# Kernel tuning notes

Measured on AMD Instinct MI355X. Metric: run time of the kernel, lower is better.

Reference implementation:

```python
import jax, jax.numpy as jnp
import numpy as np

B, S, D, H = 2, 2048, 1024, 16
HD = D // H            # head_dim = 64
CHUNK = 1024           # hard-coded in the torch module
ROPE_THETA = 10000.0


def setup_inputs() -> dict:
    key = jax.random.key(0)
    ks = jax.random.split(key, 5)
    hidden_states = jax.random.normal(ks[0], (B, S, D), dtype=jnp.float32)
    # Precomputed RoPE frequencies: freqs_cis[s, j] = exp(i * s * theta_j),
    # stored as real [S, HD//2, 2] = (cos, sin).
    inv_freq = 1.0 / (ROPE_THETA ** (np.arange(0, HD, 2, dtype=np.float32) / HD))
    ang = np.outer(np.arange(S, dtype=np.float32), inv_freq)  # [S, HD//2]
    freqs_cis = jnp.stack([jnp.cos(ang), jnp.sin(ang)], axis=-1).astype(jnp.float32)
    scale = 0.02
    Wq = jax.random.normal(ks[1], (D, D), dtype=jnp.float32) * scale
    Wk = jax.random.normal(ks[2], (D, D), dtype=jnp.float32) * scale
    Wv = jax.random.normal(ks[3], (D, D), dtype=jnp.float32) * scale
    Wo = jax.random.normal(ks[4], (D, D), dtype=jnp.float32) * scale
    return {"hidden_states": hidden_states, "freqs_cis": freqs_cis,
            "Wq": Wq, "Wk": Wk, "Wv": Wv, "Wo": Wo}


def _apply_rope(x, freqs_cis):
    # x: [B, S, H, HD]; freqs_cis: [S, HD//2, 2] (cos, sin)
    b, s, h, hd = x.shape
    xr = x.reshape(b, s, h, hd // 2, 2)
    a, bb = xr[..., 0], xr[..., 1]
    c = freqs_cis[:s, :, 0][None, :, None, :]  # broadcast over batch, heads
    d = freqs_cis[:s, :, 1][None, :, None, :]
    # complex multiply (a + ib)(c + id)
    out = jnp.stack([a * c - bb * d, a * d + bb * c], axis=-1)
    return out.reshape(b, s, h, hd)


def reference(hidden_states, freqs_cis, Wq, Wk, Wv, Wo):
    b, s, dm = hidden_states.shape
    q = (hidden_states @ Wq).reshape(b, s, H, HD)
    k = (hidden_states @ Wk).reshape(b, s, H, HD)
    v = (hidden_states @ Wv).reshape(b, s, H, HD)
    q = _apply_rope(q, freqs_cis)
    k = _apply_rope(k, freqs_cis)
    q = q.transpose(0, 2, 1, 3)  # [B, H, S, HD]
    k = k.transpose(0, 2, 1, 3)
    v = v.transpose(0, 2, 1, 3)
    scaling = HD ** (-0.5)
    out = jnp.zeros_like(q)
    # Faithful replication of the (buggy) chunked attention: softmax is
    # normalized PER key-chunk, then chunk outputs are summed.
    for i in range(0, s, CHUNK):
        j = min(i + CHUNK, s)
        w = jnp.einsum('bhqd,bhkd->bhqk', q, k[:, :, i:j]) * scaling
        w = jax.nn.softmax(w.astype(jnp.float32), axis=-1).astype(q.dtype)
        out = out + jnp.einsum('bhqk,bhkd->bhqd', w, v[:, :, i:j])
    out = out.transpose(0, 2, 1, 3).reshape(b, s, dm)
    return out @ Wo
```

## Files before the change

kernel.cpp:

```cpp
#include <hip/hip_runtime.h>
#include <hip/hip_bf16.h>
#include <cstdint>

typedef __bf16 bf16x8 __attribute__((ext_vector_type(8)));
typedef float f32x4 __attribute__((ext_vector_type(4)));
typedef float f32x16 __attribute__((ext_vector_type(16)));

#define MFMA16(a, b, c) __builtin_amdgcn_mfma_f32_16x16x32_bf16(a, b, c, 0, 0, 0)
#define MFMA32(a, b, c) __builtin_amdgcn_mfma_f32_32x32x16_bf16(a, b, c, 0, 0, 0)

__device__ __forceinline__ void gload_lds16(const void* g, void* l) {
  __builtin_amdgcn_global_load_lds(
      (const __attribute__((address_space(1))) unsigned int*)g,
      (__attribute__((address_space(3))) unsigned int*)l, 16, 0, 0);
}

__device__ __forceinline__ unsigned short f2bf(float x) {
  union { float f; uint32_t u; } v; v.f = x;
  uint32_t r = v.u + 0x7fff + ((v.u >> 16) & 1);
  return (unsigned short)(r >> 16);
}
__device__ __forceinline__ float bf2f(unsigned short h) {
  union { float f; uint32_t u; } v; v.u = ((uint32_t)h) << 16;
  return v.f;
}
__device__ __forceinline__ f32x16 fzero16() {
  f32x16 v;
#pragma unroll
  for (int i = 0; i < 16; ++i) v[i] = 0.f;
  return v;
}

__device__ __forceinline__ void ptrans(const f32x16& sv, float& rsum,
                                       bf16x8& f0, bf16x8& f1) {
  float ps[16];
#pragma unroll
  for (int r = 0; r < 16; ++r) ps[r] = __builtin_exp2f(sv[r]);
  float rs = 0.f;
#pragma unroll
  for (int r = 0; r < 16; ++r) rs += ps[r];
  rsum += rs;
  bf16x8 a, b;
#pragma unroll
  for (int r = 0; r < 8; ++r) a[r] = (__bf16)ps[r];
#pragma unroll
  for (int r = 0; r < 8; ++r) b[r] = (__bf16)ps[8 + r];
  f0 = a; f1 = b;
}

__global__ __launch_bounds__(256) void k_split(const float* __restrict__ x,
                                               unsigned short* __restrict__ hi, int n4) {
  int i = blockIdx.x * blockDim.x + threadIdx.x;
  if (i >= n4) return;
  float4 v = ((const float4*)x)[i];
  ushort4 h;
  h.x = f2bf(v.x); h.y = f2bf(v.y); h.z = f2bf(v.z); h.w = f2bf(v.w);
  ((ushort4*)hi)[i] = h;
}

__global__ __launch_bounds__(256) void k_wsplit(
    const float* __restrict__ Wq, const float* __restrict__ Wk,
    const float* __restrict__ Wv, const float* __restrict__ Wo,
    unsigned short* __restrict__ WtqH, unsigned short* __restrict__ WtkH,
    unsigned short* __restrict__ WtvH, unsigned short* __restrict__ WtoH) {
  const int z = blockIdx.z;
  const float* W = (z == 0) ? Wq : (z == 1) ? Wk : (z == 2) ? Wv : Wo;
  unsigned short* WtH = (z == 0) ? WtqH : (z == 1) ? WtkH : (z == 2) ? WtvH : WtoH;
  __shared__ float tile[32][33];
  const int bx = blockIdx.x, by = blockIdx.y;
  const int tx = threadIdx.x & 31, ty = threadIdx.x >> 5;
#pragma unroll
  for (int i = 0; i < 4; ++i)
    tile[ty + i * 8][tx] = W[(size_t)(by * 32 + ty + i * 8) * 1024 + bx * 32 + tx];
  __syncthreads();
#pragma unroll
  for (int i = 0; i < 4; ++i) {
    float v = tile[tx][ty + i * 8];
    WtH[(size_t)(bx * 32 + ty + i * 8) * 1024 + by * 32 + tx] = f2bf(v);
  }
}

__global__ __launch_bounds__(256, 2) void k_qkv(
    const unsigned short* __restrict__ hsH,
    const unsigned short* __restrict__ WqH, const unsigned short* __restrict__ WkH,
    const unsigned short* __restrict__ WvH, const float* __restrict__ freqs,
    unsigned short* __restrict__ qB, unsigned short* __restrict__ kB,
    unsigned short* __restrict__ vB) {
  __shared__ unsigned short Ah[128 * 32], Bh[128 * 32];
  const int tid = threadIdx.x;
  const int bm = blockIdx.y, bn = blockIdx.x;
  const int w = bn >> 3;
  const int n0 = (bn & 7) * 128;
  const unsigned short* WH = (w == 0) ? WqH : (w == 1) ? WkH : WvH;
  const int lane = tid & 63, wave = tid >> 6;
  const int wm = (wave & 1) * 64, wn = (wave >> 1) * 64;
  const int l15 = lane & 15, lq = lane >> 4;

  f32x4 acc[4][4];
#pragma unroll
  for (int i = 0; i < 4; i++)
#pragma unroll
    for (int j = 0; j < 4; j++) acc[i][j] = (f32x4){0.f, 0.f, 0.f, 0.f};

  const char* baseA = (const char*)hsH + (size_t)(bm * 128) * 2048;
  const char* baseB = (const char*)WH + (size_t)n0 * 2048;
  const int off0 = tid << 4, row0 = off0 >> 6, seg0 = off0 & 63;
  const int off1 = (tid + 256) << 4, row1 = off1 >> 6, seg1 = off1 & 63;

  for (int k0 = 0; k0 < 1024; k0 += 32) {
    __syncthreads();
    gload_lds16(baseA + (size_t)row0 * 2048 + k0 * 2 + seg0, (char*)Ah + wave * 1024);
    gload_lds16(baseB + (size_t)row0 * 2048 + k0 * 2 + seg0, (char*)Bh + wave * 1024);
    gload_lds16(baseA + (size_t)row1 * 2048 + k0 * 2 + seg1,
                (char*)Ah + 4096 + wave * 1024);
    gload_lds16(baseB + (size_t)row1 * 2048 + k0 * 2 + seg1,
                (char*)Bh + 4096 + wave * 1024);
    __syncthreads();
    bf16x8 ah[4], bh[4];
#pragma unroll
    for (int i = 0; i < 4; ++i) {
      ah[i] = *(const bf16x8*)&Ah[(wm + i * 16 + l15) * 32 + lq * 8];
      bh[i] = *(const bf16x8*)&Bh[(wn + i * 16 + l15) * 32 + lq * 8];
    }
#pragma unroll
    for (int i = 0; i < 4; ++i)
#pragma unroll
      for (int j = 0; j < 4; ++j) acc[i][j] = MFMA16(ah[i], bh[j], acc[i][j]);
  }

  unsigned short* dst = (w == 0) ? qB : (w == 1) ? kB : vB;
#pragma unroll
  for (int i = 0; i < 4; ++i) {
#pragma unroll
    for (int j = 0; j < 4; ++j) {
      int colw = n0 + wn + j * 16 + l15;
      int h = colw >> 6, d = colw & 63;
#pragma unroll
      for (int r = 0; r < 4; ++r) {
        int rowg = bm * 128 + wm + i * 16 + lq * 4 + r;
        int s = rowg & 2047, b = rowg >> 11;
        float val = acc[i][j][r];
        size_t bhb = (size_t)(b * 16 + h) * 131072;
        if (w < 2) {
          float partner = __shfl_xor(val, 1);
          int jj = d >> 1;
          float cs = freqs[(s * 32 + jj) * 2 + 0];
          float sn = freqs[(s * 32 + jj) * 2 + 1];
          float res = (d & 1) ? (partner * sn + val * cs) : (val * cs - partner * sn);
          if (w == 0) {
            res *= 0.18033688011112042f;
            dst[(((size_t)(b * 16 + h)) * 2048 + s) * 64 + d] = f2bf(res);
          } else {
            size_t off = (size_t)(s >> 10) * 65536 + ((s >> 6) & 15) * 4096 +
                         ((s >> 5) & 1) * 2048 + (d >> 4) * 512 +
                         ((s & 31) + 32 * ((d >> 3) & 1)) * 8 + (d & 7);
            dst[bhb + off] = f2bf(res);
          }
        } else {
          int sp = (s & ~12) | ((s & 4) << 1) | ((s & 8) >> 1);
          size_t off = (size_t)(sp >> 10) * 65536 + ((sp >> 6) & 15) * 4096 +
                       (d >> 5) * 2048 + ((sp >> 4) & 3) * 512 +
                       ((d & 31) + 32 * ((sp >> 3) & 1)) * 8 + (sp & 7);
          dst[bhb + off] = f2bf(val);
        }
      }
    }
  }
}

__global__ __launch_bounds__(256, 2) void k_attn(
    const unsigned short* __restrict__ qB, const unsigned short* __restrict__ kB,
    const unsigned short* __restrict__ vB,
    unsigned short* __restrict__ c0, unsigned short* __restrict__ c1) {
  const int tid = threadIdx.x, lane = tid & 63, wave = tid >> 6;
  const int l31 = lane & 31, lh = lane >> 5;
  const int bid = blockIdx.x;
  const int x = (bid >> 3) & 7;
  const int gg = (bid & 7) + 8 * (bid >> 6);
  const int bh = gg & 31;
  const int chunk = gg >> 5;
  const int q0 = x * 256 + wave * 64;
  const size_t base = (size_t)bh * 131072;

  bf16x8 qf[2][4];
#pragma unroll
  for (int qt = 0; qt < 2; ++qt)
#pragma unroll
    for (int ks = 0; ks < 4; ++ks)
      qf[qt][ks] = *(const bf16x8*)(qB + base + (size_t)(q0 + qt * 32 + l31) * 64 +
                                    ks * 16 + lh * 8);

  const unsigned short* kp = kB + base + chunk * 65536 + lane * 8;
  const unsigned short* vp = vB + base + chunk * 65536 + lane * 8;

  bf16x8 kfa[4], kfb[4];
#pragma unroll
  for (int ks = 0; ks < 4; ++ks) {
    kfa[ks] = *(const bf16x8*)(kp + ks * 512);
    kfb[ks] = *(const bf16x8*)(kp + 2048 + ks * 512);
  }
  kp += 4096;

  f32x16 o[2][2];
#pragma unroll
  for (int a = 0; a < 2; ++a)
#pragma unroll
    for (int bq = 0; bq < 2; ++bq) o[a][bq] = fzero16();
  float rsum[2] = {0.f, 0.f};

  for (int kb = 0; kb < 16; ++kb) {
    bf16x8 vf[2][4];
#pragma unroll
    for (int dt = 0; dt < 2; ++dt)
#pragma unroll
      for (int ks = 0; ks < 4; ++ks)
        vf[dt][ks] = *(const bf16x8*)(vp + dt * 2048 + ks * 512);

    f32x16 sA0 = fzero16(), sA1 = fzero16();
    f32x16 sB0 = fzero16(), sB1 = fzero16();
    __builtin_amdgcn_s_setprio(1);
#pragma unroll
    for (int ks = 0; ks < 4; ++ks) {
      sA0 = MFMA32(kfa[ks], qf[0][ks], sA0);
      sA1 = MFMA32(kfa[ks], qf[1][ks], sA1);
    }
#pragma unroll
    for (int ks = 0; ks < 4; ++ks) {
      sB0 = MFMA32(kfb[ks], qf[0][ks], sB0);
      sB1 = MFMA32(kfb[ks], qf[1][ks], sB1);
    }
    __builtin_amdgcn_s_setprio(0);
#pragma unroll
    for (int ks = 0; ks < 4; ++ks) kfa[ks] = *(const bf16x8*)(kp + ks * 512);
#pragma unroll
    for (int ks = 0; ks < 4; ++ks)
      kfb[ks] = *(const bf16x8*)(kp + 2048 + ks * 512);

    bf16x8 fA00, fA01, fA10, fA11;
    ptrans(sA0, rsum[0], fA00, fA01);
    ptrans(sA1, rsum[1], fA10, fA11);
    __builtin_amdgcn_s_setprio(1);
    o[0][0] = MFMA32(vf[0][0], fA00, o[0][0]);
    o[1][0] = MFMA32(vf[1][0], fA00, o[1][0]);
    o[0][0] = MFMA32(vf[0][1], fA01, o[0][0]);
    o[1][0] = MFMA32(vf[1][1], fA01, o[1][0]);
    o[0][1] = MFMA32(vf[0][0], fA10, o[0][1]);
    o[1][1] = MFMA32(vf[1][0], fA10, o[1][1]);
    o[0][1] = MFMA32(vf[0][1], fA11, o[0][1]);
    o[1][1] = MFMA32(vf[1][1], fA11, o[1][1]);
    __builtin_amdgcn_s_setprio(0);
    bf16x8 fB00, fB01, fB10, fB11;
    ptrans(sB0, rsum[0], fB00, fB01);
    ptrans(sB1, rsum[1], fB10, fB11);
    __builtin_amdgcn_s_setprio(1);
    o[0][0] = MFMA32(vf[0][2], fB00, o[0][0]);
    o[1][0] = MFMA32(vf[1][2], fB00, o[1][0]);
    o[0][0] = MFMA32(vf[0][3], fB01, o[0][0]);
    o[1][0] = MFMA32(vf[1][3], fB01, o[1][0]);
    o[0][1] = MFMA32(vf[0][2], fB10, o[0][1]);
    o[1][1] = MFMA32(vf[1][2], fB10, o[1][1]);
    o[0][1] = MFMA32(vf[0][3], fB11, o[0][1]);
    o[1][1] = MFMA32(vf[1][3], fB11, o[1][1]);
    __builtin_amdgcn_s_setprio(0);

    kp += 4096;
    vp += 4096;
  }

  unsigned short* cB = chunk ? c1 : c0;
  const int b = bh >> 4, h = bh & 15;
#pragma unroll
  for (int qt = 0; qt < 2; ++qt) {
    float lsum = rsum[qt] + __shfl_xor(rsum[qt], 32);
    float inv = 1.f / lsum;
    int s = q0 + qt * 32 + l31;
#pragma unroll
    for (int dt = 0; dt < 2; ++dt)
#pragma unroll
      for (int g = 0; g < 4; ++g) {
        int d = dt * 32 + 4 * lh + 8 * g;
        size_t idx = ((size_t)(b * 2048 + s)) * 1024 + h * 64 + d;
        ushort4 hv;
#pragma unroll
        for (int t = 0; t < 4; ++t)
          ((unsigned short*)&hv)[t] = f2bf(o[dt][qt][g * 4 + t] * inv);
        *(ushort4*)(cB + idx) = hv;
      }
  }
}

__global__ __launch_bounds__(256) void k_comb(const unsigned short* __restrict__ c0,
                                              const unsigned short* __restrict__ c1,
                                              unsigned short* __restrict__ outB,
                                              int n8) {
  int i = blockIdx.x * blockDim.x + threadIdx.x;
  if (i >= n8) return;
  uint4 a = ((const uint4*)c0)[i];
  uint4 b = ((const uint4*)c1)[i];
  uint4 r;
  const unsigned short* pa = (const unsigned short*)&a;
  const unsigned short* pb = (const unsigned short*)&b;
  unsigned short* pr = (unsigned short*)&r;
#pragma unroll
  for (int j = 0; j < 8; ++j) pr[j] = f2bf(bf2f(pa[j]) + bf2f(pb[j]));
  ((uint4*)outB)[i] = r;
}

__global__ __launch_bounds__(256, 2) void k_out(const unsigned short* __restrict__ A,
                                                const unsigned short* __restrict__ B,
                                                float* __restrict__ out) {
  __shared__ unsigned short Ah[128 * 32], Bh[128 * 32];
  const int tid = threadIdx.x;
  const int bm = blockIdx.y, n0 = blockIdx.x * 128;
  const int lane = tid & 63, wave = tid >> 6;
  const int wm = (wave & 1) * 64, wn = (wave >> 1) * 64;
  const int l15 = lane & 15, lq = lane >> 4;

  f32x4 acc[4][4];
#pragma unroll
  for (int i = 0; i < 4; i++)
#pragma unroll
    for (int j = 0; j < 4; j++) acc[i][j] = (f32x4){0.f, 0.f, 0.f, 0.f};

  const char* baseA = (const char*)A + (size_t)(bm * 128) * 2048;
  const char* baseB = (const char*)B + (size_t)n0 * 2048;
  const int off0 = tid << 4, row0 = off0 >> 6, seg0 = off0 & 63;
  const int off1 = (tid + 256) << 4, row1 = off1 >> 6, seg1 = off1 & 63;

  for (int k0 = 0; k0 < 1024; k0 += 32) {
    __syncthreads();
    gload_lds16(baseA + (size_t)row0 * 2048 + k0 * 2 + seg0, (char*)Ah + wave * 1024);
    gload_lds16(baseB + (size_t)row0 * 2048 + k0 * 2 + seg0, (char*)Bh + wave * 1024);
    gload_lds16(baseA + (size_t)row1 * 2048 + k0 * 2 + seg1,
                (char*)Ah + 4096 + wave * 1024);
    gload_lds16(baseB + (size_t)row1 * 2048 + k0 * 2 + seg1,
                (char*)Bh + 4096 + wave * 1024);
    __syncthreads();
    bf16x8 ah[4], bh[4];
#pragma unroll
    for (int i = 0; i < 4; ++i) {
      ah[i] = *(const bf16x8*)&Ah[(wm + i * 16 + l15) * 32 + lq * 8];
      bh[i] = *(const bf16x8*)&Bh[(wn + i * 16 + l15) * 32 + lq * 8];
    }
#pragma unroll
    for (int i = 0; i < 4; ++i)
#pragma unroll
      for (int j = 0; j < 4; ++j) acc[i][j] = MFMA16(ah[i], bh[j], acc[i][j]);
  }
#pragma unroll
  for (int i = 0; i < 4; ++i)
#pragma unroll
    for (int j = 0; j < 4; ++j) {
      int colw = n0 + wn + j * 16 + l15;
#pragma unroll
      for (int r = 0; r < 4; ++r) {
        int rowg = bm * 128 + wm + i * 16 + lq * 4 + r;
        out[(size_t)rowg * 1024 + colw] = acc[i][j][r];
      }
    }
}

extern "C" void kernel_launch(void* const* d_in, const int* in_sizes, int n_in,
                              void* d_out, int out_size, void* d_ws, size_t ws_size,
                              hipStream_t stream) {
  const float* hs = (const float*)d_in[0];
  const float* freqs = (const float*)d_in[1];
  const float* Wq = (const float*)d_in[2];
  const float* Wk = (const float*)d_in[3];
  const float* Wv = (const float*)d_in[4];
  const float* Wo = (const float*)d_in[5];
  float* out = (float*)d_out;

  const size_t MD = (size_t)4096 * 1024;
  const size_t WW = (size_t)1024 * 1024;
  unsigned short* hsH = (unsigned short*)d_ws;
  unsigned short* WtqH = hsH + MD;
  unsigned short* WtkH = WtqH + WW;
  unsigned short* WtvH = WtkH + WW;
  unsigned short* WtoH = WtvH + WW;
  unsigned short* qB = WtoH + WW;
  unsigned short* kB = qB + MD;
  unsigned short* vB = kB + MD;
  unsigned short* c0 = vB + MD;
  unsigned short* c1 = c0 + MD;
  unsigned short* attnB = hsH;

  k_split<<<4096, 256, 0, stream>>>(hs, hsH, (int)(MD / 4));
  k_wsplit<<<dim3(32, 32, 4), 256, 0, stream>>>(Wq, Wk, Wv, Wo,
                                                WtqH, WtkH, WtvH, WtoH);
  k_qkv<<<dim3(24, 32), 256, 0, stream>>>(hsH, WtqH, WtkH, WtvH, freqs, qB, kB, vB);
  k_attn<<<512, 256, 0, stream>>>(qB, kB, vB, c0, c1);
  k_comb<<<2048, 256, 0, stream>>>(c0, c1, attnB, (int)(MD / 8));
  k_out<<<dim3(8, 32), 256, 0, stream>>>(attnB, WtoH, out);
}
```

Measured before the change: 211.7 us.

## Stage K/V tiles through double-buffered LDS via async global-to-LDS loads

The attention kernel previously had every wave load its K and V fragments directly from global memory. Now each block cooperatively prefetches the next 64-key K/V tile into a double-buffered shared-memory region with global_load_lds, and waves read their fragments from LDS. This shares each tile across the four waves and overlaps the next tile's load with current compute. The cost is a block-wide barrier every iteration and 32KB of LDS per block, which may limit occupancy. The RoPE frequency fetch is also merged into a single float2 load.

```diff
diff --git a/kernel.cpp b/kernel.cpp
--- a/kernel.cpp
+++ b/kernel.cpp
@@ -144,8 +144,8 @@
         if (w < 2) {
           float partner = __shfl_xor(val, 1);
           int jj = d >> 1;
-          float cs = freqs[(s * 32 + jj) * 2 + 0];
-          float sn = freqs[(s * 32 + jj) * 2 + 1];
+          float2 cssn = ((const float2*)freqs)[s * 32 + jj];
+          float cs = cssn.x, sn = cssn.y;
           float res = (d & 1) ? (partner * sn + val * cs) : (val * cs - partner * sn);
           if (w == 0) {
             res *= 0.18033688011112042f;
@@ -172,6 +172,7 @@
     const unsigned short* __restrict__ qB, const unsigned short* __restrict__ kB,
     const unsigned short* __restrict__ vB,
     unsigned short* __restrict__ c0, unsigned short* __restrict__ c1) {
+  __shared__ unsigned short KV[2][8192];
   const int tid = threadIdx.x, lane = tid & 63, wave = tid >> 6;
   const int l31 = lane & 31, lh = lane >> 5;
   const int bid = blockIdx.x;
@@ -190,16 +191,14 @@
       qf[qt][ks] = *(const bf16x8*)(qB + base + (size_t)(q0 + qt * 32 + l31) * 64 +
                                     ks * 16 + lh * 8);
 
-  const unsigned short* kp = kB + base + chunk * 65536 + lane * 8;
-  const unsigned short* vp = vB + base + chunk * 65536 + lane * 8;
-
-  bf16x8 kfa[4], kfb[4];
-#pragma unroll
-  for (int ks = 0; ks < 4; ++ks) {
-    kfa[ks] = *(const bf16x8*)(kp + ks * 512);
-    kfb[ks] = *(const bf16x8*)(kp + 2048 + ks * 512);
-  }
-  kp += 4096;
+  const unsigned short* kblk = kB + base + chunk * 65536;
+  const unsigned short* vblk = vB + base + chunk * 65536;
+
+  gload_lds16((const char*)kblk + tid * 16, (char*)KV[0] + wave * 1024);
+  gload_lds16((const char*)kblk + 4096 + tid * 16, (char*)KV[0] + 4096 + wave * 1024);
+  gload_lds16((const char*)vblk + tid * 16, (char*)KV[0] + 8192 + wave * 1024);
+  gload_lds16((const char*)vblk + 4096 + tid * 16, (char*)KV[0] + 12288 + wave * 1024);
+  __syncthreads();
 
   f32x16 o[2][2];
 #pragma unroll
@@ -209,12 +208,24 @@
   float rsum[2] = {0.f, 0.f};
 
   for (int kb = 0; kb < 16; ++kb) {
-    bf16x8 vf[2][4];
-#pragma unroll
-    for (int dt = 0; dt < 2; ++dt)
-#pragma unroll
-      for (int ks = 0; ks < 4; ++ks)
-        vf[dt][ks] = *(const bf16x8*)(vp + dt * 2048 + ks * 512);
+    const unsigned short* Kc = KV[kb & 1];
+    const unsigned short* Vc = KV[kb & 1] + 4096;
+    if (kb < 15) {
+      const char* ks_ = (const char*)(kblk + (kb + 1) * 4096);
+      const char* vs_ = (const char*)(vblk + (kb + 1) * 4096);
+      char* db = (char*)KV[(kb + 1) & 1];
+      gload_lds16(ks_ + tid * 16, db + wave * 1024);
+      gload_lds16(ks_ + 4096 + tid * 16, db + 4096 + wave * 1024);
+      gload_lds16(vs_ + tid * 16, db + 8192 + wave * 1024);
+      gload_lds16(vs_ + 4096 + tid * 16, db + 12288 + wave * 1024);
+    }
+
+    bf16x8 kfa[4], kfb[4];
+#pragma unroll
+    for (int ks = 0; ks < 4; ++ks) {
+      kfa[ks] = *(const bf16x8*)(Kc + ks * 512 + lane * 8);
+      kfb[ks] = *(const bf16x8*)(Kc + 2048 + ks * 512 + lane * 8);
+    }
 
     f32x16 sA0 = fzero16(), sA1 = fzero16();
     f32x16 sB0 = fzero16(), sB1 = fzero16();
@@ -230,11 +241,13 @@
       sB1 = MFMA32(kfb[ks], qf[1][ks], sB1);
     }
     __builtin_amdgcn_s_setprio(0);
-#pragma unroll
-    for (int ks = 0; ks < 4; ++ks) kfa[ks] = *(const bf16x8*)(kp + ks * 512);
-#pragma unroll
-    for (int ks = 0; ks < 4; ++ks)
-      kfb[ks] = *(const bf16x8*)(kp + 2048 + ks * 512);
+
+    bf16x8 vf[2][4];
+#pragma unroll
+    for (int dt = 0; dt < 2; ++dt)
+#pragma unroll
+      for (int ks = 0; ks < 4; ++ks)
+        vf[dt][ks] = *(const bf16x8*)(Vc + dt * 2048 + ks * 512 + lane * 8);
 
     bf16x8 fA00, fA01, fA10, fA11;
     ptrans(sA0, rsum[0], fA00, fA01);
@@ -263,8 +276,7 @@
     o[1][1] = MFMA32(vf[1][3], fB11, o[1][1]);
     __builtin_amdgcn_s_setprio(0);
 
-    kp += 4096;
-    vp += 4096;
+    __syncthreads();
   }
 
   unsigned short* cB = chunk ? c1 : c0;
```

Result: no change. 213.4 us (+0.8%).
